# Kernel optimization log

Measured on AMD Instinct MI355X. Metric: run time of the kernel, lower is better.

Reference implementation:

```python
import jax, jax.numpy as jnp
import numpy as np

B, S, D, H, V, C = 4, 2048, 1024, 16, 32000, 10
FFN_DIM = 2 * D
HD = D // H
SCALE = float(np.sqrt(HD))


def _posenc(seq, d):
    pos = jnp.arange(seq, dtype=jnp.float32)[:, None]
    div = jnp.exp(jnp.arange(0, d, 2, dtype=jnp.float32) * (-np.log(10000.0) / d))
    pe = jnp.zeros((seq, d), dtype=jnp.float32)
    pe = pe.at[:, 0::2].set(jnp.sin(pos * div))
    pe = pe.at[:, 1::2].set(jnp.cos(pos * div))
    return pe


def _layernorm(x, g, b, eps=1e-5):
    mu = jnp.mean(x, axis=-1, keepdims=True)
    var = jnp.mean(jnp.square(x - mu), axis=-1, keepdims=True)
    return (x - mu) * jax.lax.rsqrt(var + eps) * g + b


def setup_inputs() -> dict:
    key = jax.random.key(0)
    ks = jax.random.split(key, 10)
    x_ids = jax.random.randint(ks[0], (B, S), 0, V, dtype=jnp.int64 if jax.config.jax_enable_x64 else jnp.int32)
    mask = jnp.ones((B, S), dtype=jnp.int32)
    emb = (jax.random.normal(ks[1], (V, D), jnp.float32) * 0.02).at[0].set(0.0)  # padding_idx=0
    qkv_w = jax.random.normal(ks[2], (3 * D, D), jnp.float32) * 0.02
    fc_w = jax.random.normal(ks[3], (D, D), jnp.float32) * 0.02
    fc_b = jnp.zeros((D,), jnp.float32)
    ln1_g = jnp.ones((D,), jnp.float32); ln1_b = jnp.zeros((D,), jnp.float32)
    ffn_w1 = jax.random.normal(ks[4], (FFN_DIM, D), jnp.float32) * 0.02
    ffn_b1 = jnp.zeros((FFN_DIM,), jnp.float32)
    ffn_w2 = jax.random.normal(ks[5], (D, FFN_DIM), jnp.float32) * 0.02
    ffn_b2 = jnp.zeros((D,), jnp.float32)
    ln2_g = jnp.ones((D,), jnp.float32); ln2_b = jnp.zeros((D,), jnp.float32)
    pr_w1 = jax.random.normal(ks[6], (D, D), jnp.float32) * 0.02
    pr_b1 = jnp.zeros((D,), jnp.float32)
    pr_w2 = jax.random.normal(ks[7], (C, D), jnp.float32) * 0.02
    pr_b2 = jnp.zeros((C,), jnp.float32)
    return dict(x_ids=x_ids, mask=mask, emb=emb, qkv_w=qkv_w, fc_w=fc_w, fc_b=fc_b,
                ln1_g=ln1_g, ln1_b=ln1_b, ffn_w1=ffn_w1, ffn_b1=ffn_b1,
                ffn_w2=ffn_w2, ffn_b2=ffn_b2, ln2_g=ln2_g, ln2_b=ln2_b,
                pr_w1=pr_w1, pr_b1=pr_b1, pr_w2=pr_w2, pr_b2=pr_b2)


def reference(x_ids, mask, emb, qkv_w, fc_w, fc_b, ln1_g, ln1_b,
              ffn_w1, ffn_b1, ffn_w2, ffn_b2, ln2_g, ln2_b,
              pr_w1, pr_b1, pr_w2, pr_b2):
    # embedding + absolute positional encoding
    x = emb[x_ids] + _posenc(S, D)  # [B,S,D]
    residual = x
    # multi-head attention (dropout is identity at eval)
    qkv = jnp.einsum('bsd,ed->bse', x, qkv_w)  # [B,S,3D]
    q, k, v = jnp.split(qkv, 3, axis=-1)
    q = q.reshape(B, S, H, HD)
    k = k.reshape(B, S, H, HD)
    v = v.reshape(B, S, H, HD)
    attn = jnp.einsum('bqhd,bkhd->bhqk', q, k) / SCALE  # [B,H,S,S]
    attn = jnp.where(mask[:, None, None, :] == 0, -jnp.inf, attn)
    attn = jax.nn.softmax(attn, axis=-1)
    o = jnp.einsum('bhqk,bkhd->bqhd', attn, v).reshape(B, S, D)
    o = jnp.einsum('bsd,ed->bse', o, fc_w) + fc_b
    x = _layernorm(o + residual, ln1_g, ln1_b)
    # FFN block (residual + LayerNorm inside)
    h = jax.nn.gelu(jnp.einsum('bsd,fd->bsf', x, ffn_w1) + ffn_b1, approximate=False)
    h = jnp.einsum('bsf,df->bsd', h, ffn_w2) + ffn_b2
    x = _layernorm(h + x, ln2_g, ln2_b)
    # masked max-pool over sequence
    x = jnp.where(mask[:, :, None] == 0, -jnp.inf, x).max(axis=1)  # [B,D]
    # prediction head
    h = jax.nn.gelu(x @ pr_w1.T + pr_b1, approximate=False)
    logits = h @ pr_w2.T + pr_b2  # [B,C]
    return logits
```

## Files before the change

kernel.cpp:

```cpp
#include <hip/hip_runtime.h>
#include <math.h>

#define B_   4
#define S_   2048
#define D_   1024
#define H_   16
#define HD_  64
#define C_   10
#define FFN_ 2048
#define M_   (B_ * S_)
#define D3_  (3 * D_)

typedef unsigned short u16;
typedef __bf16 bf16x8 __attribute__((ext_vector_type(8)));
typedef float  f32x4  __attribute__((ext_vector_type(4)));

#define EXPSCL 0.18033688011112042f

__device__ __forceinline__ u16 f2bf(float f) {
  union { float f; unsigned u; } x; x.f = f;
  unsigned r = x.u + 0x7fffu + ((x.u >> 16) & 1u);
  return (u16)(r >> 16);
}
__device__ __forceinline__ unsigned cvtpk(float lo, float hi) {
  unsigned r;
  asm("v_cvt_pk_bf16_f32 %0, %1, %2" : "=v"(r) : "v"(lo), "v"(hi));
  return r;
}
__device__ __forceinline__ float gelu_f(float x) {
  return 0.5f * x * (1.f + erff(x * 0.70710678118654752440f));
}
__device__ __forceinline__ void gload_lds16(const void* g, void* l) {
  __builtin_amdgcn_global_load_lds(
      (const __attribute__((address_space(1))) unsigned int*)g,
      (__attribute__((address_space(3))) unsigned int*)l, 16, 0, 0);
}
__device__ __forceinline__ bf16x8 ldsfrag(const u16* buf, int rowbase, int fr, int kb) {
  return *(const bf16x8*)&buf[(rowbase + fr) * 64 + ((kb ^ (fr & 7)) << 3)];
}

#define CV0 786432
#define CV1 262144
#define CV2 524288
#define CV3 524288
__global__ __launch_bounds__(256) void prep_kernel(const float* __restrict__ s0,
                                                   const float* __restrict__ s1,
                                                   const float* __restrict__ s2,
                                                   const float* __restrict__ s3,
                                                   u16* __restrict__ d0,
                                                   u16* __restrict__ d1,
                                                   u16* __restrict__ d2,
                                                   u16* __restrict__ d3,
                                                   const int* __restrict__ ids,
                                                   const float* __restrict__ emb,
                                                   float* __restrict__ resid,
                                                   u16* __restrict__ xb) {
  if (blockIdx.x < 8192) {
    int v = blockIdx.x * 256 + threadIdx.x;
    const float* s; u16* d;
    if (v < CV0) { s = s0; d = d0; }
    else if (v < CV0 + CV1) { s = s1; d = d1; v -= CV0; }
    else if (v < CV0 + CV1 + CV2) { s = s2; d = d2; v -= CV0 + CV1; }
    else { s = s3; d = d3; v -= CV0 + CV1 + CV2; }
    const int i = v * 4;
    f32x4 x = *(const f32x4*)&s[i];
    ushort4 o;
    o.x = f2bf(x[0]); o.y = f2bf(x[1]); o.z = f2bf(x[2]); o.w = f2bf(x[3]);
    *(ushort4*)&d[i] = o;
  } else {
    const int m  = blockIdx.x - 8192;
    const int s  = m & (S_ - 1);
    const int id = ids[m];
    const int d4 = threadIdx.x * 4;
    const f32x4 e = *(const f32x4*)&emb[(size_t)id * D_ + d4];
    const float fs = (float)s;
    const float f0 = __expf((float)d4 * (-9.210340371976184f / 1024.0f));
    const float f1 = __expf((float)(d4 + 2) * (-9.210340371976184f / 1024.0f));
    float s0v, c0v, s1v, c1v;
    __sincosf(fs * f0, &s0v, &c0v);
    __sincosf(fs * f1, &s1v, &c1v);
    f32x4 v;
    v[0] = e[0] + s0v; v[1] = e[1] + c0v; v[2] = e[2] + s1v; v[3] = e[3] + c1v;
    *(f32x4*)&resid[(size_t)m * D_ + d4] = v;
    ushort4 pk;
    pk.x = f2bf(v[0]); pk.y = f2bf(v[1]); pk.z = f2bf(v[2]); pk.w = f2bf(v[3]);
    *(ushort4*)&xb[(size_t)m * D_ + d4] = pk;
  }
}

template <int BIAS, int GELU, int OUTBF, int QSCALE, int VSPLIT>
__global__ __launch_bounds__(256) void gemm_bt(const u16* __restrict__ A,
                                               const u16* __restrict__ W,
                                               const float* __restrict__ bias,
                                               float* __restrict__ outf,
                                               u16* __restrict__ outb,
                                               u16* __restrict__ vtout,
                                               int M, int N, int K) {
  __shared__ u16 As[128 * 64];
  __shared__ u16 Bs[128 * 64];
  const int tid  = threadIdx.x;
  const int lane = tid & 63;
  const int w    = tid >> 6;
  const int nx  = gridDim.x;
  const int nwg = nx * gridDim.y;
  int t = blockIdx.y * nx + blockIdx.x;
  t = (t & 7) * (nwg >> 3) + (t >> 3);
  const int bx = t % nx, by = t / nx;
  const int l3   = lane >> 3;
  const int sb   = (lane & 7) ^ l3;
  const u16* Ag0 = A + (size_t)(by * 128 + w * 32 + l3) * K + sb * 8;
  const u16* Wg0 = W + (size_t)(bx * 128 + w * 32 + l3) * K + sb * 8;

  f32x4 acc[4][4] = {};
  const int wr  = (w & 1) * 64;
  const int wc  = (w >> 1) * 64;
  const int fr  = lane & 15;
  const int fq  = lane >> 4;

  for (int kt = 0; kt < K; kt += 64) {
#pragma unroll
    for (int c = 0; c < 4; ++c) {
      gload_lds16(Ag0 + (size_t)(c * 8) * K + kt, &As[(w * 32 + c * 8) * 64]);
      gload_lds16(Wg0 + (size_t)(c * 8) * K + kt, &Bs[(w * 32 + c * 8) * 64]);
    }
    __syncthreads();
#pragma unroll
    for (int ks = 0; ks < 2; ++ks) {
      const int kb = ks * 4 + fq;
      bf16x8 af[4], bfr[4];
#pragma unroll
      for (int i = 0; i < 4; ++i) af[i] = ldsfrag(As, wr + i * 16, fr, kb);
#pragma unroll
      for (int j = 0; j < 4; ++j) bfr[j] = ldsfrag(Bs, wc + j * 16, fr, kb);
#pragma unroll
      for (int i = 0; i < 4; ++i)
#pragma unroll
        for (int j = 0; j < 4; ++j)
          acc[i][j] = __builtin_amdgcn_mfma_f32_16x16x32_bf16(bfr[j], af[i], acc[i][j], 0, 0, 0);
    }
    __syncthreads();
  }

  const float qs = (QSCALE && bx < 8) ? EXPSCL : 1.f;
#pragma unroll
  for (int i = 0; i < 4; ++i) {
    const int m = by * 128 + wr + i * 16 + fr;
#pragma unroll
    for (int j = 0; j < 4; ++j) {
      const int nb = bx * 128 + wc + j * 16 + fq * 4;
      f32x4 v = acc[i][j];
      if (BIAS) v += *(const f32x4*)&bias[nb];
      if (GELU) {
        v[0] = gelu_f(v[0]); v[1] = gelu_f(v[1]);
        v[2] = gelu_f(v[2]); v[3] = gelu_f(v[3]);
      }
      if (QSCALE) v *= qs;
      if (VSPLIT && bx >= 16) {
        const int hh = (nb - 2 * D_) >> 6;
        const int dl = (nb - 2 * D_) & 63;
        const int bb = m >> 11, ss = m & (S_ - 1);
        u16* vdst = vtout + ((size_t)((bb * H_ + hh) * 64 + dl)) * S_ + ss;
        vdst[0]          = f2bf(v[0]);
        vdst[(size_t)S_]     = f2bf(v[1]);
        vdst[(size_t)2 * S_] = f2bf(v[2]);
        vdst[(size_t)3 * S_] = f2bf(v[3]);
      } else if (OUTBF) {
        ushort4 pk;
        pk.x = f2bf(v[0]); pk.y = f2bf(v[1]); pk.z = f2bf(v[2]); pk.w = f2bf(v[3]);
        *(ushort4*)&outb[(size_t)m * N + nb] = pk;
      } else {
        *(f32x4*)&outf[(size_t)m * N + nb] = v;
      }
    }
  }
}

__global__ __launch_bounds__(256) void attn_mfma_kernel(const u16* __restrict__ qkv,
                                                        const u16* __restrict__ vt,
                                                        const int* __restrict__ mask,
                                                        u16* __restrict__ attno) {
  __shared__ u16 Ks[64 * 64];
  __shared__ u16 Vts[64 * 64];
  __shared__ u16 Ps[4][32 * 64];
  const int tid = threadIdx.x, lane = tid & 63, w = tid >> 6;
  int t = (blockIdx.z * 16 + blockIdx.y) * 16 + blockIdx.x;
  t = (t & 7) * 128 + (t >> 3);
  const int qt = t & 15, h = (t >> 4) & 15, b = t >> 8;
  const int l3 = lane >> 3;
  const int sb = (lane & 7) ^ l3;
  const int fr = lane & 15, fq = lane >> 4;
  u16* PsFlat = &Ps[0][0];

  {
    const u16* qbase = qkv + (size_t)(b * S_ + qt * 128 + w * 32) * D3_ + h * 64 + sb * 8;
#pragma unroll
    for (int c = 0; c < 4; ++c)
      gload_lds16(qbase + (size_t)(c * 8 + l3) * D3_, &PsFlat[(w * 32 + c * 8) * 64]);
  }

  bool ALLV;
  {
    const int4* mp = (const int4*)&mask[b * S_];
    int mv = 1;
#pragma unroll
    for (int tt = 0; tt < 8; ++tt) {
      const int4 m4 = mp[tt * 64 + lane];
      mv &= (m4.x != 0) & (m4.y != 0) & (m4.z != 0) & (m4.w != 0);
    }
    ALLV = (__ballot(mv != 0) == ~0ull);
  }

  __syncthreads();

  bf16x8 qf[2][2];
#pragma unroll
  for (int ks = 0; ks < 2; ++ks)
#pragma unroll
    for (int i = 0; i < 2; ++i)
      qf[ks][i] = ldsfrag(PsFlat, w * 32 + i * 16, fr, ks * 4 + fq);

  __syncthreads();

  bf16x8 onesf;
#pragma unroll
  for (int k = 0; k < 8; ++k) onesf[k] = (__bf16)1.0f;

  f32x4 ot[4][2] = {};
  f32x4 otl[2] = {};
  u16* PsW = Ps[w];

  for (int kt = 0; kt < S_ / 64; ++kt) {
    {
      const u16* kbase = qkv + (size_t)(b * S_ + kt * 64 + w * 16) * D3_ + D_ + h * 64 + sb * 8;
      gload_lds16(kbase + (size_t)l3 * D3_, &Ks[(w * 16) * 64]);
      gload_lds16(kbase + (size_t)(8 + l3) * D3_, &Ks[(w * 16 + 8) * 64]);
      const u16* vbase = vt + ((size_t)((b * H_ + h) * 64 + w * 16)) * S_ + kt * 64 + sb * 8;
      gload_lds16(vbase + (size_t)l3 * S_, &Vts[(w * 16) * 64]);
      gload_lds16(vbase + (size_t)(8 + l3) * S_, &Vts[(w * 16 + 8) * 64]);
    }
    __syncthreads();

    f32x4 sf[4][2] = {};
#pragma unroll
    for (int ks = 0; ks < 2; ++ks) {
      const int kb = ks * 4 + fq;
      __builtin_amdgcn_s_setprio(1);
#pragma unroll
      for (int r4 = 0; r4 < 4; ++r4) {
        bf16x8 kf = ldsfrag(Ks, r4 * 16, fr, kb);
        sf[r4][0] = __builtin_amdgcn_mfma_f32_16x16x32_bf16(kf, qf[ks][0], sf[r4][0], 0, 0, 0);
        sf[r4][1] = __builtin_amdgcn_mfma_f32_16x16x32_bf16(kf, qf[ks][1], sf[r4][1], 0, 0, 0);
      }
      __builtin_amdgcn_s_setprio(0);
    }
    if (!ALLV) {
#pragma unroll
      for (int r4 = 0; r4 < 4; ++r4) {
        const int4 mm = *(const int4*)&mask[b * S_ + kt * 64 + r4 * 16 + fq * 4];
        f32x4 vb;
        vb[0] = mm.x ? 0.f : -1e30f;
        vb[1] = mm.y ? 0.f : -1e30f;
        vb[2] = mm.z ? 0.f : -1e30f;
        vb[3] = mm.w ? 0.f : -1e30f;
        sf[r4][0] += vb;
        sf[r4][1] += vb;
      }
    }

#pragma unroll
    for (int i = 0; i < 2; ++i) {
      const int prow = i * 16 + fr;
      u16* pw = PsW + prow * 64;
#pragma unroll
      for (int r4 = 0; r4 < 4; ++r4) {
        const float p0 = __builtin_exp2f(sf[r4][i][0]);
        const float p1 = __builtin_exp2f(sf[r4][i][1]);
        const float p2 = __builtin_exp2f(sf[r4][i][2]);
        const float p3 = __builtin_exp2f(sf[r4][i][3]);
        const int bk0 = 2 * r4 + (fq >> 1);
        const int off = ((bk0 ^ (prow & 7)) << 3) + ((fq & 1) << 2);
        uint2 pk; pk.x = cvtpk(p0, p1); pk.y = cvtpk(p2, p3);
        *(uint2*)&pw[off] = pk;
      }
    }
    asm volatile("s_waitcnt lgkmcnt(0)" ::: "memory");

#pragma unroll
    for (int ks = 0; ks < 2; ++ks) {
      const int kb = ks * 4 + fq;
      bf16x8 pf0 = ldsfrag(PsW, 0, fr, kb);
      bf16x8 pf1 = ldsfrag(PsW, 16, fr, kb);
      __builtin_amdgcn_s_setprio(1);
#pragma unroll
      for (int db = 0; db < 4; ++db) {
        bf16x8 vf = ldsfrag(Vts, db * 16, fr, kb);
        ot[db][0] = __builtin_amdgcn_mfma_f32_16x16x32_bf16(vf, pf0, ot[db][0], 0, 0, 0);
        ot[db][1] = __builtin_amdgcn_mfma_f32_16x16x32_bf16(vf, pf1, ot[db][1], 0, 0, 0);
      }
      otl[0] = __builtin_amdgcn_mfma_f32_16x16x32_bf16(onesf, pf0, otl[0], 0, 0, 0);
      otl[1] = __builtin_amdgcn_mfma_f32_16x16x32_bf16(onesf, pf1, otl[1], 0, 0, 0);
      __builtin_amdgcn_s_setprio(0);
    }
    __syncthreads();
  }

#pragma unroll
  for (int i = 0; i < 2; ++i) {
    const float l = otl[i][0];
    const float inv = (l > 0.f) ? 1.f / l : 0.f;
    const int qrow = qt * 128 + w * 32 + i * 16 + fr;
    u16* dst = attno + (size_t)(b * S_ + qrow) * D_ + h * 64 + fq * 4;
#pragma unroll
    for (int db = 0; db < 4; ++db) {
      ushort4 pk;
      pk.x = f2bf(ot[db][i][0] * inv);
      pk.y = f2bf(ot[db][i][1] * inv);
      pk.z = f2bf(ot[db][i][2] * inv);
      pk.w = f2bf(ot[db][i][3] * inv);
      *(ushort4*)&dst[db * 16] = pk;
    }
  }
}

template <int WRITEB>
__global__ __launch_bounds__(256) void ln_kernel(const float* __restrict__ a,
                                                 const float* __restrict__ res,
                                                 const float* __restrict__ g,
                                                 const float* __restrict__ be,
                                                 float* __restrict__ outf,
                                                 u16* __restrict__ outb) {
  const int row = blockIdx.x, tid = threadIdx.x;
  const int lane = tid & 63, w = tid >> 6;
  const size_t base = (size_t)row * D_ + tid * 4;
  const f32x4 va = *(const f32x4*)(a + base);
  const f32x4 vr = *(const f32x4*)(res + base);
  const f32x4 v  = va + vr;
  float s = v[0] + v[1] + v[2] + v[3];
#pragma unroll
  for (int o = 32; o > 0; o >>= 1) s += __shfl_xor(s, o);
  __shared__ float red[8];
  if (lane == 0) red[w] = s;
  __syncthreads();
  const float mu = (red[0] + red[1] + red[2] + red[3]) * (1.f / D_);
  const f32x4 d = v - mu;
  float s2 = d[0] * d[0] + d[1] * d[1] + d[2] * d[2] + d[3] * d[3];
#pragma unroll
  for (int o = 32; o > 0; o >>= 1) s2 += __shfl_xor(s2, o);
  if (lane == 0) red[4 + w] = s2;
  __syncthreads();
  const float var = (red[4] + red[5] + red[6] + red[7]) * (1.f / D_);
  const float rs = rsqrtf(var + 1e-5f);
  f32x4 y;
#pragma unroll
  for (int k = 0; k < 4; ++k) {
    const int ch = tid * 4 + k;
    y[k] = d[k] * rs * g[ch] + be[ch];
  }
  *(f32x4*)&outf[base] = y;
  if (WRITEB) {
    ushort4 pk;
    pk.x = f2bf(y[0]); pk.y = f2bf(y[1]); pk.z = f2bf(y[2]); pk.w = f2bf(y[3]);
    *(ushort4*)&outb[base] = pk;
  }
}

__global__ __launch_bounds__(256) void pool_part_kernel(const float* __restrict__ x,
                                                        const int* __restrict__ mask,
                                                        float* __restrict__ part) {
  const int b = blockIdx.y, ch = blockIdx.x;
  const int d0 = threadIdx.x * 4;
  f32x4 acc = {-INFINITY, -INFINITY, -INFINITY, -INFINITY};
  for (int ss = 0; ss < 64; ++ss) {
    const int s = ch * 64 + ss;
    if (mask[b * S_ + s] != 0) {
      const f32x4 v = *(const f32x4*)&x[(size_t)(b * S_ + s) * D_ + d0];
      acc[0] = fmaxf(acc[0], v[0]);
      acc[1] = fmaxf(acc[1], v[1]);
      acc[2] = fmaxf(acc[2], v[2]);
      acc[3] = fmaxf(acc[3], v[3]);
    }
  }
  *(f32x4*)&part[(size_t)(b * 32 + ch) * D_ + d0] = acc;
}
__global__ __launch_bounds__(256) void pool_final_kernel(const float* __restrict__ part,
                                                         float* __restrict__ pooled) {
  const int b = blockIdx.x;
  const int d0 = threadIdx.x * 4;
  f32x4 acc = {-INFINITY, -INFINITY, -INFINITY, -INFINITY};
  for (int ch = 0; ch < 32; ++ch) {
    const f32x4 v = *(const f32x4*)&part[(size_t)(b * 32 + ch) * D_ + d0];
    acc[0] = fmaxf(acc[0], v[0]);
    acc[1] = fmaxf(acc[1], v[1]);
    acc[2] = fmaxf(acc[2], v[2]);
    acc[3] = fmaxf(acc[3], v[3]);
  }
  *(f32x4*)&pooled[(size_t)b * D_ + d0] = acc;
}

__global__ __launch_bounds__(256) void head1_kernel(const float* __restrict__ pooled,
                                                    const float* __restrict__ w,
                                                    const float* __restrict__ bias,
                                                    float* __restrict__ hh) {
  const int lane = threadIdx.x & 63;
  const int gw = blockIdx.x * 4 + (threadIdx.x >> 6);
  const int b = gw >> 10, n = gw & 1023;
  const float* p  = pooled + b * 1024;
  const float* wr = w + (size_t)n * 1024;
  float s = 0.f;
  for (int d = lane; d < 1024; d += 64) s += p[d] * wr[d];
#pragma unroll
  for (int off = 32; off > 0; off >>= 1) s += __shfl_xor(s, off);
  if (lane == 0) hh[b * 1024 + n] = gelu_f(s + bias[n]);
}
__global__ __launch_bounds__(256) void head2_kernel(const float* __restrict__ hh,
                                                    const float* __restrict__ w,
                                                    const float* __restrict__ bias,
                                                    float* __restrict__ out) {
  const int lane = threadIdx.x & 63;
  const int gw = blockIdx.x * 4 + (threadIdx.x >> 6);
  const int b = gw / 10, c = gw % 10;
  const float* p  = hh + b * 1024;
  const float* wr = w + (size_t)c * 1024;
  float s = 0.f;
  for (int d = lane; d < 1024; d += 64) s += p[d] * wr[d];
#pragma unroll
  for (int off = 32; off > 0; off >>= 1) s += __shfl_xor(s, off);
  if (lane == 0) out[b * 10 + c] = s + bias[c];
}

#define OFF_RESID  0UL
#define OFF_F1     33554432UL
#define OFF_XB     67108864UL
#define OFF_QKVB   83886080UL
#define OFF_ATTNO  134217728UL
#define OFF_WQKV   150994944UL
#define OFF_WFC    157286400UL
#define OFF_WF1    159383552UL
#define OFF_WF2    163577856UL
#define OFF_PART   167772160UL
#define OFF_POOLED 168296448UL
#define OFF_HH     168312832UL

extern "C" void kernel_launch(void* const* d_in, const int* in_sizes, int n_in,
                              void* d_out, int out_size, void* d_ws, size_t ws_size,
                              hipStream_t stream) {
  const int*   x_ids  = (const int*)d_in[0];
  const int*   mask   = (const int*)d_in[1];
  const float* emb    = (const float*)d_in[2];
  const float* qkv_w  = (const float*)d_in[3];
  const float* fc_w   = (const float*)d_in[4];
  const float* fc_b   = (const float*)d_in[5];
  const float* ln1_g  = (const float*)d_in[6];
  const float* ln1_b  = (const float*)d_in[7];
  const float* ffn_w1 = (const float*)d_in[8];
  const float* ffn_b1 = (const float*)d_in[9];
  const float* ffn_w2 = (const float*)d_in[10];
  const float* ffn_b2 = (const float*)d_in[11];
  const float* ln2_g  = (const float*)d_in[12];
  const float* ln2_b  = (const float*)d_in[13];
  const float* pr_w1  = (const float*)d_in[14];
  const float* pr_b1  = (const float*)d_in[15];
  const float* pr_w2  = (const float*)d_in[16];
  const float* pr_b2  = (const float*)d_in[17];
  float* out = (float*)d_out;
  char* ws = (char*)d_ws;

  float* resid  = (float*)(ws + OFF_RESID);
  float* f1     = (float*)(ws + OFF_F1);
  u16*   vtb    = (u16*)(ws + OFF_F1);
  u16*   xb     = (u16*)(ws + OFF_XB);
  u16*   qkvb   = (u16*)(ws + OFF_QKVB);
  u16*   hb     = (u16*)(ws + OFF_QKVB);
  u16*   attnob = (u16*)(ws + OFF_ATTNO);
  u16*   wqkvb  = (u16*)(ws + OFF_WQKV);
  u16*   wfcb   = (u16*)(ws + OFF_WFC);
  u16*   wf1b   = (u16*)(ws + OFF_WF1);
  u16*   wf2b   = (u16*)(ws + OFF_WF2);
  float* part   = (float*)(ws + OFF_PART);
  float* pooled = (float*)(ws + OFF_POOLED);
  float* hh     = (float*)(ws + OFF_HH);

  prep_kernel<<<16384, 256, 0, stream>>>(qkv_w, fc_w, ffn_w1, ffn_w2,
                                         wqkvb, wfcb, wf1b, wf2b,
                                         x_ids, emb, resid, xb);

  gemm_bt<0, 0, 1, 1, 1><<<dim3(D3_ / 128, M_ / 128), 256, 0, stream>>>(
      xb, wqkvb, nullptr, nullptr, qkvb, vtb, M_, D3_, D_);

  attn_mfma_kernel<<<dim3(S_ / 128, H_, B_), 256, 0, stream>>>(qkvb, vtb, mask, attnob);

  gemm_bt<1, 0, 0, 0, 0><<<dim3(D_ / 128, M_ / 128), 256, 0, stream>>>(
      attnob, wfcb, fc_b, f1, nullptr, nullptr, M_, D_, D_);

  ln_kernel<1><<<M_, 256, 0, stream>>>(f1, resid, ln1_g, ln1_b, resid, xb);

  gemm_bt<1, 1, 1, 0, 0><<<dim3(FFN_ / 128, M_ / 128), 256, 0, stream>>>(
      xb, wf1b, ffn_b1, nullptr, hb, nullptr, M_, FFN_, D_);

  gemm_bt<1, 0, 0, 0, 0><<<dim3(D_ / 128, M_ / 128), 256, 0, stream>>>(
      hb, wf2b, ffn_b2, f1, nullptr, nullptr, M_, D_, FFN_);

  ln_kernel<0><<<M_, 256, 0, stream>>>(f1, resid, ln2_g, ln2_b, f1, nullptr);

  pool_part_kernel<<<dim3(32, B_), 256, 0, stream>>>(f1, mask, part);
  pool_final_kernel<<<B_, 256, 0, stream>>>(part, pooled);

  head1_kernel<<<1024, 256, 0, stream>>>(pooled, pr_w1, pr_b1, hh);
  head2_kernel<<<10, 256, 0, stream>>>(hh, pr_w2, pr_b2, out);
}
```

Baseline: 591.2 us.

## Split attention block into 8 waves of 16 query rows, compute row sums in VALU

The attention kernel now launches 512 threads per block, with each of 8 waves handling 16 query rows instead of 32. Each thread's K/V tile load is halved to match. The softmax denominator was computed with an extra MFMA against a ones vector; it is now summed in registers and reduced with cross-lane shuffles. This aims for more waves in flight and fewer MFMAs per wave, at the cost of each K/V fragment read from LDS being reused across only one query sub-tile instead of two.

```diff
diff --git a/kernel.cpp b/kernel.cpp
--- a/kernel.cpp
+++ b/kernel.cpp
@@ -175,13 +175,13 @@
   }
 }
 
-__global__ __launch_bounds__(256) void attn_mfma_kernel(const u16* __restrict__ qkv,
+__global__ __launch_bounds__(512) void attn_mfma_kernel(const u16* __restrict__ qkv,
                                                         const u16* __restrict__ vt,
                                                         const int* __restrict__ mask,
                                                         u16* __restrict__ attno) {
   __shared__ u16 Ks[64 * 64];
   __shared__ u16 Vts[64 * 64];
-  __shared__ u16 Ps[4][32 * 64];
+  __shared__ u16 Ps[8][16 * 64];
   const int tid = threadIdx.x, lane = tid & 63, w = tid >> 6;
   int t = (blockIdx.z * 16 + blockIdx.y) * 16 + blockIdx.x;
   t = (t & 7) * 128 + (t >> 3);
@@ -192,10 +192,9 @@
   u16* PsFlat = &Ps[0][0];
 
   {
-    const u16* qbase = qkv + (size_t)(b * S_ + qt * 128 + w * 32) * D3_ + h * 64 + sb * 8;
-#pragma unroll
-    for (int c = 0; c < 4; ++c)
-      gload_lds16(qbase + (size_t)(c * 8 + l3) * D3_, &PsFlat[(w * 32 + c * 8) * 64]);
+    const u16* qbase = qkv + (size_t)(b * S_ + qt * 128 + w * 16) * D3_ + h * 64 + sb * 8;
+    gload_lds16(qbase + (size_t)l3 * D3_, &PsFlat[(w * 16) * 64]);
+    gload_lds16(qbase + (size_t)(8 + l3) * D3_, &PsFlat[(w * 16 + 8) * 64]);
   }
 
   bool ALLV;
@@ -212,35 +211,27 @@
 
   __syncthreads();
 
-  bf16x8 qf[2][2];
+  bf16x8 qf[2];
 #pragma unroll
   for (int ks = 0; ks < 2; ++ks)
-#pragma unroll
-    for (int i = 0; i < 2; ++i)
-      qf[ks][i] = ldsfrag(PsFlat, w * 32 + i * 16, fr, ks * 4 + fq);
+    qf[ks] = ldsfrag(PsFlat, w * 16, fr, ks * 4 + fq);
 
   __syncthreads();
 
-  bf16x8 onesf;
-#pragma unroll
-  for (int k = 0; k < 8; ++k) onesf[k] = (__bf16)1.0f;
-
-  f32x4 ot[4][2] = {};
-  f32x4 otl[2] = {};
+  float l_st = 0.f;
+  f32x4 ot[4] = {};
   u16* PsW = Ps[w];
 
   for (int kt = 0; kt < S_ / 64; ++kt) {
     {
-      const u16* kbase = qkv + (size_t)(b * S_ + kt * 64 + w * 16) * D3_ + D_ + h * 64 + sb * 8;
-      gload_lds16(kbase + (size_t)l3 * D3_, &Ks[(w * 16) * 64]);
-      gload_lds16(kbase + (size_t)(8 + l3) * D3_, &Ks[(w * 16 + 8) * 64]);
-      const u16* vbase = vt + ((size_t)((b * H_ + h) * 64 + w * 16)) * S_ + kt * 64 + sb * 8;
-      gload_lds16(vbase + (size_t)l3 * S_, &Vts[(w * 16) * 64]);
-      gload_lds16(vbase + (size_t)(8 + l3) * S_, &Vts[(w * 16 + 8) * 64]);
+      const u16* kbase = qkv + (size_t)(b * S_ + kt * 64 + w * 8 + l3) * D3_ + D_ + h * 64 + sb * 8;
+      gload_lds16(kbase, &Ks[(w * 8) * 64]);
+      const u16* vbase = vt + ((size_t)((b * H_ + h) * 64 + w * 8 + l3)) * S_ + kt * 64 + sb * 8;
+      gload_lds16(vbase, &Vts[(w * 8) * 64]);
     }
     __syncthreads();
 
-    f32x4 sf[4][2] = {};
+    f32x4 sf[4] = {};
 #pragma unroll
     for (int ks = 0; ks < 2; ++ks) {
       const int kb = ks * 4 + fq;
@@ -248,8 +239,7 @@
 #pragma unroll
       for (int r4 = 0; r4 < 4; ++r4) {
         bf16x8 kf = ldsfrag(Ks, r4 * 16, fr, kb);
-        sf[r4][0] = __builtin_amdgcn_mfma_f32_16x16x32_bf16(kf, qf[ks][0], sf[r4][0], 0, 0, 0);
-        sf[r4][1] = __builtin_amdgcn_mfma_f32_16x16x32_bf16(kf, qf[ks][1], sf[r4][1], 0, 0, 0);
+        sf[r4] = __builtin_amdgcn_mfma_f32_16x16x32_bf16(kf, qf[ks], sf[r4], 0, 0, 0);
       }
       __builtin_amdgcn_s_setprio(0);
     }
@@ -262,61 +252,58 @@
         vb[1] = mm.y ? 0.f : -1e30f;
         vb[2] = mm.z ? 0.f : -1e30f;
         vb[3] = mm.w ? 0.f : -1e30f;
-        sf[r4][0] += vb;
-        sf[r4][1] += vb;
-      }
-    }
-
-#pragma unroll
-    for (int i = 0; i < 2; ++i) {
-      const int prow = i * 16 + fr;
-      u16* pw = PsW + prow * 64;
+        sf[r4] += vb;
+      }
+    }
+
+    {
+      u16* pw = PsW + fr * 64;
+      float sum = l_st;
 #pragma unroll
       for (int r4 = 0; r4 < 4; ++r4) {
-        const float p0 = __builtin_exp2f(sf[r4][i][0]);
-        const float p1 = __builtin_exp2f(sf[r4][i][1]);
-        const float p2 = __builtin_exp2f(sf[r4][i][2]);
-        const float p3 = __builtin_exp2f(sf[r4][i][3]);
+        const float p0 = __builtin_exp2f(sf[r4][0]);
+        const float p1 = __builtin_exp2f(sf[r4][1]);
+        const float p2 = __builtin_exp2f(sf[r4][2]);
+        const float p3 = __builtin_exp2f(sf[r4][3]);
+        sum += (p0 + p1) + (p2 + p3);
         const int bk0 = 2 * r4 + (fq >> 1);
-        const int off = ((bk0 ^ (prow & 7)) << 3) + ((fq & 1) << 2);
+        const int off = ((bk0 ^ (fr & 7)) << 3) + ((fq & 1) << 2);
         uint2 pk; pk.x = cvtpk(p0, p1); pk.y = cvtpk(p2, p3);
         *(uint2*)&pw[off] = pk;
       }
+      l_st = sum;
     }
     asm volatile("s_waitcnt lgkmcnt(0)" ::: "memory");
 
 #pragma unroll
     for (int ks = 0; ks < 2; ++ks) {
       const int kb = ks * 4 + fq;
-      bf16x8 pf0 = ldsfrag(PsW, 0, fr, kb);
-      bf16x8 pf1 = ldsfrag(PsW, 16, fr, kb);
+      bf16x8 pf = ldsfrag(PsW, 0, fr, kb);
       __builtin_amdgcn_s_setprio(1);
 #pragma unroll
       for (int db = 0; db < 4; ++db) {
         bf16x8 vf = ldsfrag(Vts, db * 16, fr, kb);
-        ot[db][0] = __builtin_amdgcn_mfma_f32_16x16x32_bf16(vf, pf0, ot[db][0], 0, 0, 0);
-        ot[db][1] = __builtin_amdgcn_mfma_f32_16x16x32_bf16(vf, pf1, ot[db][1], 0, 0, 0);
-      }
-      otl[0] = __builtin_amdgcn_mfma_f32_16x16x32_bf16(onesf, pf0, otl[0], 0, 0, 0);
-      otl[1] = __builtin_amdgcn_mfma_f32_16x16x32_bf16(onesf, pf1, otl[1], 0, 0, 0);
+        ot[db] = __builtin_amdgcn_mfma_f32_16x16x32_bf16(vf, pf, ot[db], 0, 0, 0);
+      }
       __builtin_amdgcn_s_setprio(0);
     }
     __syncthreads();
   }
 
-#pragma unroll
-  for (int i = 0; i < 2; ++i) {
-    const float l = otl[i][0];
+  {
+    float l = l_st;
+    l += __shfl_xor(l, 16);
+    l += __shfl_xor(l, 32);
     const float inv = (l > 0.f) ? 1.f / l : 0.f;
-    const int qrow = qt * 128 + w * 32 + i * 16 + fr;
+    const int qrow = qt * 128 + w * 16 + fr;
     u16* dst = attno + (size_t)(b * S_ + qrow) * D_ + h * 64 + fq * 4;
 #pragma unroll
     for (int db = 0; db < 4; ++db) {
       ushort4 pk;
-      pk.x = f2bf(ot[db][i][0] * inv);
-      pk.y = f2bf(ot[db][i][1] * inv);
-      pk.z = f2bf(ot[db][i][2] * inv);
-      pk.w = f2bf(ot[db][i][3] * inv);
+      pk.x = f2bf(ot[db][0] * inv);
+      pk.y = f2bf(ot[db][1] * inv);
+      pk.z = f2bf(ot[db][2] * inv);
+      pk.w = f2bf(ot[db][3] * inv);
       *(ushort4*)&dst[db * 16] = pk;
     }
   }
@@ -487,7 +474,7 @@
   gemm_bt<0, 0, 1, 1, 1><<<dim3(D3_ / 128, M_ / 128), 256, 0, stream>>>(
       xb, wqkvb, nullptr, nullptr, qkvb, vtb, M_, D3_, D_);
 
-  attn_mfma_kernel<<<dim3(S_ / 128, H_, B_), 256, 0, stream>>>(qkvb, vtb, mask, attnob);
+  attn_mfma_kernel<<<dim3(S_ / 128, H_, B_), 512, 0, stream>>>(qkvb, vtb, mask, attnob);
 
   gemm_bt<1, 0, 0, 0, 0><<<dim3(D_ / 128, M_ / 128), 256, 0, stream>>>(
       attnob, wfcb, fc_b, f1, nullptr, nullptr, M_, D_, D_);
```

Measured after the change: 599.1 us. About the same (+1.3%).
